# Kernel tuning notes

Hardware: AMD Instinct MI355X
Metric: run time of the kernel (lower is better)

## Reference

```python
import jax, jax.numpy as jnp
import numpy as np

LX = LZ = 64
B_BOND = 8
KCH = 3
DX = DZ = 2
N_STATES = 4
SAMPLES = 65536


def setup_inputs() -> dict:
    key = jax.random.key(0)
    k1, k2, k3, k4 = jax.random.split(key, 4)
    biadj = jax.random.normal(k1, (LX, LZ, B_BOND), dtype=jnp.float32)
    eps_ten = jax.random.normal(k2, (B_BOND, KCH, DX, DZ), dtype=jnp.float32)
    chi = jax.random.normal(k3, (N_STATES, N_STATES, KCH), dtype=jnp.float32)
    x0_idx = jax.random.randint(k4, (SAMPLES, LX * DX), 0, N_STATES)
    return {"biadj": biadj, "eps_ten": eps_ten, "chi": chi, "x0_idx": x0_idx}


def _kernel(biadj, eps_ten, chi):
    # biadj: [Lx,Lz,b], eps_ten: [b,k,dx,dz], chi: [n,n,k]
    Lx, Lz, _ = biadj.shape
    _, k, dx, dz = eps_ten.shape
    coupling = jnp.tensordot(biadj, eps_ten, axes=([2], [0]))  # [Lx,Lz,k,dx,dz]
    coupling = coupling.transpose(0, 3, 1, 4, 2).reshape(Lx * dx, Lz * dz, k)
    return jnp.tensordot(coupling, chi, axes=([2], [2]))  # [X,Z,n,n]


def reference(biadj, eps_ten, chi, x0_idx):
    """ERBM.cd_x with steps=1: one Gibbs sweep + CD loss. Returns (loss, x)."""
    n = chi.shape[0]
    K = _kernel(biadj, eps_ten, chi)  # [X,Z,n,n]
    x0 = jax.nn.one_hot(x0_idx, n, dtype=K.dtype)  # [S,X,n]
    kz, kx = jax.random.split(jax.random.key(42))
    # ez = tensordot(x0, K, dims=([1,2],[0,2])) -> [S,Z,n]
    ez = jnp.einsum('sxa,xzab->szb', x0, K)
    z = jax.nn.one_hot(jax.random.categorical(kz, -ez), n, dtype=K.dtype)
    # ex = tensordot(z, K, dims=([1,2],[1,3])) -> [S,X,n]
    ex = jnp.einsum('szb,xzab->sxa', z, K)
    x = jax.nn.one_hot(jax.random.categorical(kx, -ex), n, dtype=K.dtype)
    loss = jnp.sum(ex * (x0 - x), axis=(1, 2)).mean()
    return loss, x
```

## Files before the change

kernel.cpp:

```cpp
#include <hip/hip_runtime.h>
#include <stdint.h>

#define NS   65536
#define XD   128
#define ZD   128

typedef float f32x2 __attribute__((ext_vector_type(2)));
struct F4p { f32x2 lo, hi; };

struct U2 { uint32_t x, y; };

__host__ __device__ constexpr uint32_t rotl32(uint32_t v, int r) {
  return (v << r) | (v >> (32 - r));
}

__host__ __device__ constexpr U2 threefry2x32(uint32_t k0, uint32_t k1,
                                              uint32_t x0, uint32_t x1) {
  uint32_t ks0 = k0, ks1 = k1, ks2 = k0 ^ k1 ^ 0x1BD11BDAu;
  x0 += ks0; x1 += ks1;
  x0 += x1; x1 = rotl32(x1, 13); x1 ^= x0;
  x0 += x1; x1 = rotl32(x1, 15); x1 ^= x0;
  x0 += x1; x1 = rotl32(x1, 26); x1 ^= x0;
  x0 += x1; x1 = rotl32(x1,  6); x1 ^= x0;
  x0 += ks1; x1 += ks2 + 1u;
  x0 += x1; x1 = rotl32(x1, 17); x1 ^= x0;
  x0 += x1; x1 = rotl32(x1, 29); x1 ^= x0;
  x0 += x1; x1 = rotl32(x1, 16); x1 ^= x0;
  x0 += x1; x1 = rotl32(x1, 24); x1 ^= x0;
  x0 += ks2; x1 += ks0 + 2u;
  x0 += x1; x1 = rotl32(x1, 13); x1 ^= x0;
  x0 += x1; x1 = rotl32(x1, 15); x1 ^= x0;
  x0 += x1; x1 = rotl32(x1, 26); x1 ^= x0;
  x0 += x1; x1 = rotl32(x1,  6); x1 ^= x0;
  x0 += ks0; x1 += ks1 + 3u;
  x0 += x1; x1 = rotl32(x1, 17); x1 ^= x0;
  x0 += x1; x1 = rotl32(x1, 29); x1 ^= x0;
  x0 += x1; x1 = rotl32(x1, 16); x1 ^= x0;
  x0 += x1; x1 = rotl32(x1, 24); x1 ^= x0;
  x0 += ks1; x1 += ks2 + 4u;
  x0 += x1; x1 = rotl32(x1, 13); x1 ^= x0;
  x0 += x1; x1 = rotl32(x1, 15); x1 ^= x0;
  x0 += x1; x1 = rotl32(x1, 26); x1 ^= x0;
  x0 += x1; x1 = rotl32(x1,  6); x1 ^= x0;
  x0 += ks2; x1 += ks0 + 5u;
  return {x0, x1};
}

constexpr U2 KEYZ = threefry2x32(0u, 42u, 0u, 0u);
constexpr U2 KEYX = threefry2x32(0u, 42u, 0u, 1u);
constexpr uint32_t KZ0 = KEYZ.x, KZ1 = KEYZ.y;
constexpr uint32_t KX0 = KEYX.x, KX1 = KEYX.y;

__device__ inline float gumbel32f(uint32_t k0, uint32_t k1, uint32_t idx) {
  U2 h = threefry2x32(k0, k1, 0u, idx);
  uint32_t bits = h.x ^ h.y;
  float f = __uint_as_float((bits >> 9) | 0x3f800000u) - 1.0f;
  float u = fmaxf(f, 1.1754943508222875e-38f);
  float lu = __logf(u);
  return -__logf(-lu);
}

struct Acc { double v0, v1, v2, v3; };

__device__ inline double pick(const Acc& d, int i) {
  return (i == 0) ? d.v0 : (i == 1) ? d.v1 : (i == 2) ? d.v2 : d.v3;
}

__device__ inline int argmax4(double v0, double v1, double v2, double v3) {
  int best = 0; double bv = v0;
  if (v1 > bv) { bv = v1; best = 1; }
  if (v2 > bv) { bv = v2; best = 2; }
  if (v3 > bv) { bv = v3; best = 3; }
  return best;
}

__device__ inline int sample4(uint32_t k0, uint32_t k1, uint32_t ib, const Acc& d) {
  return argmax4((double)gumbel32f(k0, k1, ib + 0u) - d.v0,
                 (double)gumbel32f(k0, k1, ib + 1u) - d.v1,
                 (double)gumbel32f(k0, k1, ib + 2u) - d.v2,
                 (double)gumbel32f(k0, k1, ib + 3u) - d.v3);
}

__global__ __launch_bounds__(256) void init_fused(const int* __restrict__ x0,
                                                  const float* __restrict__ biadj,
                                                  const float* __restrict__ eps,
                                                  const float* __restrict__ chi,
                                                  uint32_t* __restrict__ pk,
                                                  float* __restrict__ Kz,
                                                  float* __restrict__ Kx) {
  if (blockIdx.x < 2048) {
    int t = blockIdx.x * 256 + threadIdx.x;
    const int4* src = (const int4*)x0 + (size_t)t * 4;
    uint32_t w = 0;
#pragma unroll
    for (int i = 0; i < 4; ++i) {
      int4 v = src[i];
      w |= (uint32_t)(v.x & 3) << (8 * i + 0);
      w |= (uint32_t)(v.y & 3) << (8 * i + 2);
      w |= (uint32_t)(v.z & 3) << (8 * i + 4);
      w |= (uint32_t)(v.w & 3) << (8 * i + 6);
    }
    pk[t] = w;
  } else {
    int t = (blockIdx.x - 2048) * 256 + threadIdx.x;
    int xx = t >> 7, zz = t & 127;
    int ix = xx >> 1, dx = xx & 1;
    int iz = zz >> 1, dz = zz & 1;
    double c0 = 0.0, c1 = 0.0, c2 = 0.0;
#pragma unroll
    for (int b = 0; b < 8; ++b) {
      double bi = (double)biadj[(ix * 64 + iz) * 8 + b];
      c0 += bi * (double)eps[((b * 3 + 0) * 2 + dx) * 2 + dz];
      c1 += bi * (double)eps[((b * 3 + 1) * 2 + dx) * 2 + dz];
      c2 += bi * (double)eps[((b * 3 + 2) * 2 + dx) * 2 + dz];
    }
#pragma unroll
    for (int p = 0; p < 4; ++p)
#pragma unroll
      for (int q = 0; q < 4; ++q) {
        double kv = c0 * (double)chi[(p * 4 + q) * 3 + 0]
                  + c1 * (double)chi[(p * 4 + q) * 3 + 1]
                  + c2 * (double)chi[(p * 4 + q) * 3 + 2];
        float kf = (float)kv;
        Kz[((zz * 128 + xx) * 4 + p) * 4 + q] = kf;
        Kx[((xx * 128 + zz) * 4 + q) * 4 + p] = kf;
      }
  }
}

__global__ __launch_bounds__(256) void build_pairs(const float* __restrict__ Kz,
                                                   const float* __restrict__ Kx,
                                                   float4* __restrict__ PZ,
                                                   float4* __restrict__ PX) {
  int gid = blockIdx.x * 256 + threadIdx.x;
  int isX = gid >> 17;
  int t = gid & 131071;
  int c = t & 15, rp = (t >> 4) & 63, r = t >> 10;
  const float4* K4 = (const float4*)(isX ? Kx : Kz);
  float4 kA = K4[(r * 128 + 2 * rp) * 4 + (c & 3)];
  float4 kB = K4[(r * 128 + 2 * rp + 1) * 4 + (c >> 2)];
  float4* P = isX ? PX : PZ;
  P[(r * 64 + rp) * 16 + c] =
      float4{kA.x + kB.x, kA.y + kB.y, kA.z + kB.z, kA.w + kB.w};
}

__device__ inline void pair_accum2(const F4p* __restrict__ L,
                                   const uint32_t* __restrict__ cw,
                                   Acc& dA, Acc& dB) {
#pragma unroll
  for (int g = 0; g < 4; ++g) {
    f32x2 a01 = {0.f, 0.f}, a23 = {0.f, 0.f};
    f32x2 b01 = {0.f, 0.f}, b23 = {0.f, 0.f};
#pragma unroll
    for (int j2 = 0; j2 < 2; ++j2) {
      uint32_t w = cw[2 * g + j2];
#pragma unroll
      for (int t = 0; t < 8; ++t) {
        int c = (w >> (4 * t)) & 15;
        const F4p* e = &L[(16 * g + 8 * j2 + t) * 16 + c];
        F4p e0 = e[0];
        F4p e1 = e[1024];
        a01 += e0.lo; a23 += e0.hi;
        b01 += e1.lo; b23 += e1.hi;
      }
    }
    dA.v0 += (double)a01.x; dA.v1 += (double)a01.y;
    dA.v2 += (double)a23.x; dA.v3 += (double)a23.y;
    dB.v0 += (double)b01.x; dB.v1 += (double)b01.y;
    dB.v2 += (double)b23.x; dB.v3 += (double)b23.y;
  }
}

__global__ __launch_bounds__(256, 5) void ez_pair(const float4* __restrict__ PZ,
                                                  const uint32_t* __restrict__ pk,
                                                  uint8_t* __restrict__ zidxT) {
  __shared__ F4p Ltab[2048];
  int tid = threadIdx.x;
  int by = blockIdx.y;
  {
    const uint4* src = (const uint4*)(PZ + (size_t)by * 2048);
    uint4* dst = (uint4*)Ltab;
#pragma unroll
    for (int i = 0; i < 8; ++i) dst[tid + i * 256] = src[tid + i * 256];
  }
  __syncthreads();
  int s = blockIdx.x * 256 + tid;
  uint32_t cw[8];
  {
    uint4 w0 = *(const uint4*)(pk + (size_t)s * 8);
    uint4 w1 = *(const uint4*)(pk + (size_t)s * 8 + 4);
    cw[0] = w0.x; cw[1] = w0.y; cw[2] = w0.z; cw[3] = w0.w;
    cw[4] = w1.x; cw[5] = w1.y; cw[6] = w1.z; cw[7] = w1.w;
  }
  Acc dA = {0, 0, 0, 0}, dB = {0, 0, 0, 0};
  pair_accum2(Ltab, cw, dA, dB);

  int z0 = 2 * by, z1 = 2 * by + 1;
  uint32_t ib = ((uint32_t)s * 128u + (uint32_t)z0) * 4u;
  zidxT[(size_t)z0 * NS + s] = (uint8_t)sample4(KZ0, KZ1, ib, dA);
  zidxT[(size_t)z1 * NS + s] = (uint8_t)sample4(KZ0, KZ1, ib + 4u, dB);
}

__global__ __launch_bounds__(256) void repack_z(const uint8_t* __restrict__ zidxT,
                                                uint32_t* __restrict__ zpk) {
  uint32_t t = blockIdx.x * 256u + threadIdx.x;
  uint32_t j = t >> 16, s = t & 65535u;
  uint32_t w = 0;
#pragma unroll
  for (int k = 0; k < 16; ++k)
    w |= (uint32_t)zidxT[(size_t)(16 * j + k) * NS + s] << (2 * k);
  zpk[t] = w;
}

__global__ __launch_bounds__(256, 5) void ex_pair(const float4* __restrict__ PX,
                                                  const uint32_t* __restrict__ zpk,
                                                  const uint32_t* __restrict__ pk,
                                                  uint8_t* __restrict__ xidxT,
                                                  double* __restrict__ loss_part) {
  __shared__ F4p Ltab[2048];
  int tid = threadIdx.x;
  int by = blockIdx.y;
  {
    const uint4* src = (const uint4*)(PX + (size_t)by * 2048);
    uint4* dst = (uint4*)Ltab;
#pragma unroll
    for (int i = 0; i < 8; ++i) dst[tid + i * 256] = src[tid + i * 256];
  }
  __syncthreads();
  int s = blockIdx.x * 256 + tid;
  uint32_t cw[8];
#pragma unroll
  for (int j = 0; j < 8; ++j) cw[j] = zpk[(size_t)j * NS + s];
  Acc dA = {0, 0, 0, 0}, dB = {0, 0, 0, 0};
  pair_accum2(Ltab, cw, dA, dB);

  int x0 = 2 * by, x1 = 2 * by + 1;
  uint32_t ib = ((uint32_t)s * 128u + (uint32_t)x0) * 4u;
  int bestA = sample4(KX0, KX1, ib, dA);
  int bestB = sample4(KX0, KX1, ib + 4u, dB);
  xidxT[(size_t)x0 * NS + s] = (uint8_t)bestA;
  xidxT[(size_t)x1 * NS + s] = (uint8_t)bestB;

  uint32_t wj = pk[(size_t)s * 8 + (x0 >> 4)];
  int aiA = (wj >> (2 * (x0 & 15))) & 3;
  int aiB = (wj >> (2 * (x1 & 15))) & 3;
  double term = pick(dA, aiA) - pick(dA, bestA)
              + pick(dB, aiB) - pick(dB, bestB);
#pragma unroll
  for (int off = 32; off > 0; off >>= 1) term += __shfl_down(term, off, 64);
  __syncthreads();
  double* red = (double*)Ltab;
  if ((tid & 63) == 0) red[tid >> 6] = term;
  __syncthreads();
  if (tid == 0)
    loss_part[(size_t)by * 256 + blockIdx.x] = red[0] + red[1] + red[2] + red[3];
}

__global__ __launch_bounds__(256) void write_out(const uint8_t* __restrict__ xidxT,
                                                 const double* __restrict__ loss_part,
                                                 float* __restrict__ out) {
  __shared__ uint8_t tile[128 * 80];
  __shared__ double red2[4];
  int tid = threadIdx.x;
  int s0 = blockIdx.x * 64;
  {
    int x = tid >> 1, chunk = tid & 1;
    const uint8_t* src = xidxT + (size_t)x * NS + s0 + chunk * 32;
    uint4 v0 = *(const uint4*)(src);
    uint4 v1 = *(const uint4*)(src + 16);
    *(uint4*)&tile[x * 80 + chunk * 32 + 0]  = v0;
    *(uint4*)&tile[x * 80 + chunk * 32 + 16] = v1;
  }
  __syncthreads();
  float4* dst = (float4*)(out + 1 + (size_t)s0 * 512);
#pragma unroll 4
  for (int k = 0; k < 32; ++k) {
    int idx = k * 256 + tid;
    int x = idx & 127, sl = idx >> 7;
    int b = tile[x * 80 + sl];
    dst[idx] = float4{b == 0 ? 1.0f : 0.0f, b == 1 ? 1.0f : 0.0f,
                      b == 2 ? 1.0f : 0.0f, b == 3 ? 1.0f : 0.0f};
  }
  if (blockIdx.x == 0) {
    double p = 0.0;
#pragma unroll 4
    for (int i = tid; i < 16384; i += 256) p += loss_part[i];
#pragma unroll
    for (int off = 32; off > 0; off >>= 1) p += __shfl_down(p, off, 64);
    if ((tid & 63) == 0) red2[tid >> 6] = p;
    __syncthreads();
    if (tid == 0)
      out[0] = (float)((red2[0] + red2[1] + red2[2] + red2[3]) * (1.0 / 65536.0));
  }
}

extern "C" void kernel_launch(void* const* d_in, const int* in_sizes, int n_in,
                              void* d_out, int out_size, void* d_ws, size_t ws_size,
                              hipStream_t stream) {
  const float* biadj = (const float*)d_in[0];
  const float* eps   = (const float*)d_in[1];
  const float* chi   = (const float*)d_in[2];
  const int*   x0    = (const int*)d_in[3];
  float* out = (float*)d_out;

  char* w = (char*)d_ws;
  double*   loss_part = (double*)w;                w += (size_t)16384 * 8;
  float*    Kz    = (float*)w;                     w += (size_t)128 * 128 * 16 * 4;
  float*    Kx    = (float*)w;                     w += (size_t)128 * 128 * 16 * 4;
  uint32_t* pk    = (uint32_t*)w;                  w += (size_t)NS * 8 * 4;
  uint8_t*  zidxT = (uint8_t*)w;                   w += (size_t)NS * ZD;
  uint32_t* zpk   = (uint32_t*)w;                  w += (size_t)NS * 8 * 4;
  uint8_t*  xidxT = (uint8_t*)w;                   w += (size_t)NS * XD;
  float4*   PZ    = (float4*)w;                    w += (size_t)128 * 64 * 16 * 16;
  float4*   PX    = (float4*)w;

  init_fused<<<2112, 256, 0, stream>>>(x0, biadj, eps, chi, pk, Kz, Kx);
  build_pairs<<<1024, 256, 0, stream>>>(Kz, Kx, PZ, PX);
  ez_pair<<<dim3(NS / 256, ZD / 2), 256, 0, stream>>>((const float4*)PZ, pk, zidxT);
  repack_z<<<NS * 8 / 256, 256, 0, stream>>>(zidxT, zpk);
  ex_pair<<<dim3(NS / 256, XD / 2), 256, 0, stream>>>((const float4*)PX, zpk, pk, xidxT, loss_part);
  write_out<<<NS / 64, 256, 0, stream>>>(xidxT, loss_part, out);
}
```

Measured before the change: 489.4 us.

## Fuse pair-table build into setup and stage only part of LDS tables

Merges the K construction and pair-table build into one setup kernel that computes the paired float4 entries directly, removing the Kz/Kx intermediate buffers and one launch. In ez_pair/ex_pair, only three quarters of the pair table is copied to shared memory (1536 entries instead of 2048); the first group of lookups reads straight from global/L2. The smaller LDS footprint allows raising launch bounds from 5 to 6 blocks per CU. The trade-off is that a quarter of the random-index lookups become uncoalesced global reads.

```diff
diff --git a/kernel.cpp b/kernel.cpp
--- a/kernel.cpp
+++ b/kernel.cpp
@@ -81,13 +81,13 @@
                  (double)gumbel32f(k0, k1, ib + 3u) - d.v3);
 }
 
-__global__ __launch_bounds__(256) void init_fused(const int* __restrict__ x0,
-                                                  const float* __restrict__ biadj,
-                                                  const float* __restrict__ eps,
-                                                  const float* __restrict__ chi,
-                                                  uint32_t* __restrict__ pk,
-                                                  float* __restrict__ Kz,
-                                                  float* __restrict__ Kx) {
+__global__ __launch_bounds__(256) void setup(const int* __restrict__ x0,
+                                             const float* __restrict__ biadj,
+                                             const float* __restrict__ eps,
+                                             const float* __restrict__ chi,
+                                             uint32_t* __restrict__ pk,
+                                             float4* __restrict__ PZ,
+                                             float4* __restrict__ PX) {
   if (blockIdx.x < 2048) {
     int t = blockIdx.x * 256 + threadIdx.x;
     const int4* src = (const int4*)x0 + (size_t)t * 4;
@@ -102,64 +102,66 @@
     }
     pk[t] = w;
   } else {
-    int t = (blockIdx.x - 2048) * 256 + threadIdx.x;
-    int xx = t >> 7, zz = t & 127;
-    int ix = xx >> 1, dx = xx & 1;
-    int iz = zz >> 1, dz = zz & 1;
-    double c0 = 0.0, c1 = 0.0, c2 = 0.0;
+    int gid = (blockIdx.x - 2048) * 256 + threadIdx.x;
+    int isX = gid >> 17;
+    int t = gid & 131071;
+    int c = t & 15, rp = (t >> 4) & 63, r = t >> 10;
+    int ixA, dxA, izA, dzA, ixB, dxB, izB, dzB;
+    if (!isX) {
+      ixA = rp; dxA = 0; ixB = rp; dxB = 1;
+      izA = r >> 1; dzA = r & 1; izB = izA; dzB = dzA;
+    } else {
+      ixA = r >> 1; dxA = r & 1; ixB = ixA; dxB = dxA;
+      izA = rp; dzA = 0; izB = rp; dzB = 1;
+    }
+    double c0A = 0.0, c1A = 0.0, c2A = 0.0, c0B = 0.0, c1B = 0.0, c2B = 0.0;
 #pragma unroll
     for (int b = 0; b < 8; ++b) {
-      double bi = (double)biadj[(ix * 64 + iz) * 8 + b];
-      c0 += bi * (double)eps[((b * 3 + 0) * 2 + dx) * 2 + dz];
-      c1 += bi * (double)eps[((b * 3 + 1) * 2 + dx) * 2 + dz];
-      c2 += bi * (double)eps[((b * 3 + 2) * 2 + dx) * 2 + dz];
-    }
-#pragma unroll
-    for (int p = 0; p < 4; ++p)
-#pragma unroll
-      for (int q = 0; q < 4; ++q) {
-        double kv = c0 * (double)chi[(p * 4 + q) * 3 + 0]
-                  + c1 * (double)chi[(p * 4 + q) * 3 + 1]
-                  + c2 * (double)chi[(p * 4 + q) * 3 + 2];
-        float kf = (float)kv;
-        Kz[((zz * 128 + xx) * 4 + p) * 4 + q] = kf;
-        Kx[((xx * 128 + zz) * 4 + q) * 4 + p] = kf;
-      }
-  }
-}
-
-__global__ __launch_bounds__(256) void build_pairs(const float* __restrict__ Kz,
-                                                   const float* __restrict__ Kx,
-                                                   float4* __restrict__ PZ,
-                                                   float4* __restrict__ PX) {
-  int gid = blockIdx.x * 256 + threadIdx.x;
-  int isX = gid >> 17;
-  int t = gid & 131071;
-  int c = t & 15, rp = (t >> 4) & 63, r = t >> 10;
-  const float4* K4 = (const float4*)(isX ? Kx : Kz);
-  float4 kA = K4[(r * 128 + 2 * rp) * 4 + (c & 3)];
-  float4 kB = K4[(r * 128 + 2 * rp + 1) * 4 + (c >> 2)];
-  float4* P = isX ? PX : PZ;
-  P[(r * 64 + rp) * 16 + c] =
-      float4{kA.x + kB.x, kA.y + kB.y, kA.z + kB.z, kA.w + kB.w};
-}
-
-__device__ inline void pair_accum2(const F4p* __restrict__ L,
-                                   const uint32_t* __restrict__ cw,
-                                   Acc& dA, Acc& dB) {
-#pragma unroll
-  for (int g = 0; g < 4; ++g) {
+      double biA = (double)biadj[(ixA * 64 + izA) * 8 + b];
+      c0A += biA * (double)eps[((b * 3 + 0) * 2 + dxA) * 2 + dzA];
+      c1A += biA * (double)eps[((b * 3 + 1) * 2 + dxA) * 2 + dzA];
+      c2A += biA * (double)eps[((b * 3 + 2) * 2 + dxA) * 2 + dzA];
+      double biB = (double)biadj[(ixB * 64 + izB) * 8 + b];
+      c0B += biB * (double)eps[((b * 3 + 0) * 2 + dxB) * 2 + dzB];
+      c1B += biB * (double)eps[((b * 3 + 1) * 2 + dxB) * 2 + dzB];
+      c2B += biB * (double)eps[((b * 3 + 2) * 2 + dxB) * 2 + dzB];
+    }
+    float out[4];
+#pragma unroll
+    for (int q = 0; q < 4; ++q) {
+      int pqA, pqB;
+      if (!isX) { pqA = (c & 3) * 4 + q; pqB = (c >> 2) * 4 + q; }
+      else      { pqA = q * 4 + (c & 3); pqB = q * 4 + (c >> 2); }
+      double kvA = c0A * (double)chi[pqA * 3 + 0]
+                 + c1A * (double)chi[pqA * 3 + 1]
+                 + c2A * (double)chi[pqA * 3 + 2];
+      double kvB = c0B * (double)chi[pqB * 3 + 0]
+                 + c1B * (double)chi[pqB * 3 + 1]
+                 + c2B * (double)chi[pqB * 3 + 2];
+      out[q] = (float)kvA + (float)kvB;
+    }
+    float4* P = isX ? PX : PZ;
+    P[(r * 64 + rp) * 16 + c] = float4{out[0], out[1], out[2], out[3]};
+  }
+}
+
+__device__ inline void pair_accum_hyb(const F4p* __restrict__ L,
+                                      const F4p* __restrict__ G0,
+                                      const F4p* __restrict__ G1,
+                                      const uint32_t* __restrict__ cw,
+                                      Acc& dA, Acc& dB) {
+  {
     f32x2 a01 = {0.f, 0.f}, a23 = {0.f, 0.f};
     f32x2 b01 = {0.f, 0.f}, b23 = {0.f, 0.f};
 #pragma unroll
     for (int j2 = 0; j2 < 2; ++j2) {
-      uint32_t w = cw[2 * g + j2];
+      uint32_t w = cw[j2];
 #pragma unroll
       for (int t = 0; t < 8; ++t) {
         int c = (w >> (4 * t)) & 15;
-        const F4p* e = &L[(16 * g + 8 * j2 + t) * 16 + c];
-        F4p e0 = e[0];
-        F4p e1 = e[1024];
+        int idx = (8 * j2 + t) * 16 + c;
+        F4p e0 = G0[idx];
+        F4p e1 = G1[idx];
         a01 += e0.lo; a23 += e0.hi;
         b01 += e1.lo; b23 += e1.hi;
       }
@@ -169,20 +171,49 @@
     dB.v0 += (double)b01.x; dB.v1 += (double)b01.y;
     dB.v2 += (double)b23.x; dB.v3 += (double)b23.y;
   }
-}
-
-__global__ __launch_bounds__(256, 5) void ez_pair(const float4* __restrict__ PZ,
+#pragma unroll
+  for (int g = 1; g < 4; ++g) {
+    f32x2 a01 = {0.f, 0.f}, a23 = {0.f, 0.f};
+    f32x2 b01 = {0.f, 0.f}, b23 = {0.f, 0.f};
+#pragma unroll
+    for (int j2 = 0; j2 < 2; ++j2) {
+      uint32_t w = cw[2 * g + j2];
+#pragma unroll
+      for (int t = 0; t < 8; ++t) {
+        int c = (w >> (4 * t)) & 15;
+        const F4p* e = &L[(16 * (g - 1) + 8 * j2 + t) * 16 + c];
+        F4p e0 = e[0];
+        F4p e1 = e[768];
+        a01 += e0.lo; a23 += e0.hi;
+        b01 += e1.lo; b23 += e1.hi;
+      }
+    }
+    dA.v0 += (double)a01.x; dA.v1 += (double)a01.y;
+    dA.v2 += (double)a23.x; dA.v3 += (double)a23.y;
+    dB.v0 += (double)b01.x; dB.v1 += (double)b01.y;
+    dB.v2 += (double)b23.x; dB.v3 += (double)b23.y;
+  }
+}
+
+__device__ inline void stage_tables(const F4p* __restrict__ Pby, F4p* __restrict__ Ltab,
+                                    int tid) {
+  const uint4* src0 = (const uint4*)(Pby + 256);
+  const uint4* src1 = (const uint4*)(Pby + 1280);
+  uint4* dst = (uint4*)Ltab;
+#pragma unroll
+  for (int i = 0; i < 3; ++i) dst[tid + i * 256] = src0[tid + i * 256];
+#pragma unroll
+  for (int i = 0; i < 3; ++i) dst[768 + tid + i * 256] = src1[tid + i * 256];
+}
+
+__global__ __launch_bounds__(256, 6) void ez_pair(const float4* __restrict__ PZ,
                                                   const uint32_t* __restrict__ pk,
                                                   uint8_t* __restrict__ zidxT) {
-  __shared__ F4p Ltab[2048];
+  __shared__ F4p Ltab[1536];
   int tid = threadIdx.x;
   int by = blockIdx.y;
-  {
-    const uint4* src = (const uint4*)(PZ + (size_t)by * 2048);
-    uint4* dst = (uint4*)Ltab;
-#pragma unroll
-    for (int i = 0; i < 8; ++i) dst[tid + i * 256] = src[tid + i * 256];
-  }
+  const F4p* Pby = (const F4p*)PZ + (size_t)by * 2048;
+  stage_tables(Pby, Ltab, tid);
   __syncthreads();
   int s = blockIdx.x * 256 + tid;
   uint32_t cw[8];
@@ -193,7 +224,7 @@
     cw[4] = w1.x; cw[5] = w1.y; cw[6] = w1.z; cw[7] = w1.w;
   }
   Acc dA = {0, 0, 0, 0}, dB = {0, 0, 0, 0};
-  pair_accum2(Ltab, cw, dA, dB);
+  pair_accum_hyb(Ltab, Pby, Pby + 1024, cw, dA, dB);
 
   int z0 = 2 * by, z1 = 2 * by + 1;
   uint32_t ib = ((uint32_t)s * 128u + (uint32_t)z0) * 4u;
@@ -212,27 +243,23 @@
   zpk[t] = w;
 }
 
-__global__ __launch_bounds__(256, 5) void ex_pair(const float4* __restrict__ PX,
+__global__ __launch_bounds__(256, 6) void ex_pair(const float4* __restrict__ PX,
                                                   const uint32_t* __restrict__ zpk,
                                                   const uint32_t* __restrict__ pk,
                                                   uint8_t* __restrict__ xidxT,
                                                   double* __restrict__ loss_part) {
-  __shared__ F4p Ltab[2048];
+  __shared__ F4p Ltab[1536];
   int tid = threadIdx.x;
   int by = blockIdx.y;
-  {
-    const uint4* src = (const uint4*)(PX + (size_t)by * 2048);
-    uint4* dst = (uint4*)Ltab;
-#pragma unroll
-    for (int i = 0; i < 8; ++i) dst[tid + i * 256] = src[tid + i * 256];
-  }
+  const F4p* Pby = (const F4p*)PX + (size_t)by * 2048;
+  stage_tables(Pby, Ltab, tid);
   __syncthreads();
   int s = blockIdx.x * 256 + tid;
   uint32_t cw[8];
 #pragma unroll
   for (int j = 0; j < 8; ++j) cw[j] = zpk[(size_t)j * NS + s];
   Acc dA = {0, 0, 0, 0}, dB = {0, 0, 0, 0};
-  pair_accum2(Ltab, cw, dA, dB);
+  pair_accum_hyb(Ltab, Pby, Pby + 1024, cw, dA, dB);
 
   int x0 = 2 * by, x1 = 2 * by + 1;
   uint32_t ib = ((uint32_t)s * 128u + (uint32_t)x0) * 4u;
@@ -305,8 +332,6 @@
 
   char* w = (char*)d_ws;
   double*   loss_part = (double*)w;                w += (size_t)16384 * 8;
-  float*    Kz    = (float*)w;                     w += (size_t)128 * 128 * 16 * 4;
-  float*    Kx    = (float*)w;                     w += (size_t)128 * 128 * 16 * 4;
   uint32_t* pk    = (uint32_t*)w;                  w += (size_t)NS * 8 * 4;
   uint8_t*  zidxT = (uint8_t*)w;                   w += (size_t)NS * ZD;
   uint32_t* zpk   = (uint32_t*)w;                  w += (size_t)NS * 8 * 4;
@@ -314,10 +339,9 @@
   float4*   PZ    = (float4*)w;                    w += (size_t)128 * 64 * 16 * 16;
   float4*   PX    = (float4*)w;
 
-  init_fused<<<2112, 256, 0, stream>>>(x0, biadj, eps, chi, pk, Kz, Kx);
-  build_pairs<<<1024, 256, 0, stream>>>(Kz, Kx, PZ, PX);
-  ez_pair<<<dim3(NS / 256, ZD / 2), 256, 0, stream>>>((const float4*)PZ, pk, zidxT);
+  setup<<<3072, 256, 0, stream>>>(x0, biadj, eps, chi, pk, PZ, PX);
+  ez_pair<<<dim3(NS / 256, ZD / 2), 256, 0, stream>>>(PZ, pk, zidxT);
   repack_z<<<NS * 8 / 256, 256, 0, stream>>>(zidxT, zpk);
-  ex_pair<<<dim3(NS / 256, XD / 2), 256, 0, stream>>>((const float4*)PX, zpk, pk, xidxT, loss_part);
+  ex_pair<<<dim3(NS / 256, XD / 2), 256, 0, stream>>>(PX, zpk, pk, xidxT, loss_part);
   write_out<<<NS / 64, 256, 0, stream>>>(xidxT, loss_part, out);
 }
```

New measurement: 471.7 us (median of 2 runs). -3.6%, faster.
